# Kernel tuning notes

Measured on AMD Instinct MI355X. Metric: run time of the kernel, lower is better.

Reference implementation:

```python
import jax, jax.numpy as jnp
import numpy as np

B, C, D = 1024, 100000, 512
S_SCALE, MARGIN, EPS = 64.0, 0.5, 1e-7  # arcface defaults


def setup_inputs() -> dict:
    key = jax.random.key(0)
    kx, kl, kw = jax.random.split(key, 3)
    x = jax.random.normal(kx, (B, D), dtype=jnp.float32)
    labels = jax.random.randint(kl, (B,), 0, C, dtype=jnp.int64)
    # nn.Linear default init: U(-1/sqrt(fan_in), 1/sqrt(fan_in))
    bound = 1.0 / np.sqrt(D)
    W = jax.random.uniform(kw, (C, D), dtype=jnp.float32, minval=-bound, maxval=bound)
    return {"x": x, "labels": labels, "W": W}


def reference(x, labels, W):
    # L2-normalize features (W is NOT normalized in the original -- the
    # normalize loop there rebinds a local and is a no-op).
    xn = x / jnp.maximum(jnp.linalg.norm(x, axis=1, keepdims=True), 1e-12)
    wf = jnp.einsum('bd,cd->bc', xn, W)               # [B, C] cosine-like logits
    target = jnp.take_along_axis(wf, labels[:, None], axis=1)[:, 0]  # [B]
    # arcface: s * cos(acos(clamp(cos_theta)) + m)
    numerator = S_SCALE * jnp.cos(
        jnp.arccos(jnp.clip(target, -1.0 + EPS, 1.0 - EPS)) + MARGIN)
    # sum over excluded classes = full sum - label term
    excl_sum = jnp.sum(jnp.exp(S_SCALE * wf), axis=1) - jnp.exp(S_SCALE * target)
    L = numerator - jnp.log(jnp.exp(numerator) + excl_sum)
    return -jnp.mean(L)
```

## Files before the change

kernel.cpp:

```cpp
#include <hip/hip_runtime.h>
#include <hip/hip_bf16.h>
#include <math.h>

#define NB 1024
#define NC 100000
#define ND 512
#define SSCALE 64.0f
#define MMARGIN 0.5f

#define BM 128
#define BN 128
#define BK 64
#define NKS (ND / BK)
#define NRT (NB / BM)
#define NCT ((NC + BN - 1) / BN)
#define GRIDSZ (NRT * NCT)

typedef __bf16 bf16x8 __attribute__((ext_vector_type(8)));
typedef float f32x4 __attribute__((ext_vector_type(4)));

__device__ __forceinline__ void gload_lds16(const void* g, void* l) {
    __builtin_amdgcn_global_load_lds(
        (const __attribute__((address_space(1))) unsigned int*)g,
        (__attribute__((address_space(3))) unsigned int*)l, 16, 0, 0);
}


__global__ void prep_kernel(const float* __restrict__ x, __bf16* __restrict__ xnb) {
    const int row = blockIdx.x;
    const int tid = threadIdx.x;
    const float2 v = *reinterpret_cast<const float2*>(x + (size_t)row * ND + tid * 2);
    float ss = v.x * v.x + v.y * v.y;
#pragma unroll
    for (int m = 1; m < 64; m <<= 1) ss += __shfl_xor(ss, m);
    __shared__ float wsum[4];
    if ((tid & 63) == 0) wsum[tid >> 6] = ss;
    __syncthreads();
    const float tot = wsum[0] + wsum[1] + wsum[2] + wsum[3];
    const float inv = 1.0f / fmaxf(sqrtf(tot), 1e-12f);
    __bf16* dst = xnb + (size_t)row * ND + tid * 2;
    dst[0] = (__bf16)(v.x * inv);
    dst[1] = (__bf16)(v.y * inv);
}

__global__ void target_kernel(const __bf16* __restrict__ xnb, const float* __restrict__ Wg,
                              const int* __restrict__ labels, float* __restrict__ tgt) {
    const int wid  = threadIdx.x >> 6;
    const int lane = threadIdx.x & 63;
    const int row  = blockIdx.x * 4 + wid;
    const int lab  = labels[row];
    const int k    = lane * 8;
    const bf16x8 xv = *reinterpret_cast<const bf16x8*>(xnb + (size_t)row * ND + k);
    const float* wr = Wg + (size_t)lab * ND + k;
    const float4 w0 = *reinterpret_cast<const float4*>(wr);
    const float4 w1 = *reinterpret_cast<const float4*>(wr + 4);
    float s = (float)xv[0] * w0.x + (float)xv[1] * w0.y + (float)xv[2] * w0.z + (float)xv[3] * w0.w
            + (float)xv[4] * w1.x + (float)xv[5] * w1.y + (float)xv[6] * w1.z + (float)xv[7] * w1.w;
#pragma unroll
    for (int m = 1; m < 64; m <<= 1) s += __shfl_xor(s, m);
    if (lane == 0) tgt[row] = s;
}

__global__ __launch_bounds__(256, 3) void gemm_exp_kernel(const __bf16* __restrict__ xnb,
                                                          const float* __restrict__ Wg,
                                                          float* __restrict__ sums) {
    __shared__ char lds[49152];
    const int tid  = threadIdx.x;
    const int wid  = tid >> 6;
    const int lane = tid & 63;
    const int l15  = lane & 15;
    const int lhi  = lane >> 4;
    const int wr   = wid >> 1;
    const int wc   = wid & 1;

    const int logical = (blockIdx.x & 7) * (GRIDSZ / 8) + (blockIdx.x >> 3);
    const int rt = logical & 7;
    const int ct = logical >> 3;
    const int r0 = rt * BM;
    const int c0 = ct * BN;

    float4 bw[8];

    const int bcls = (tid >> 3);
    const int bqp  = tid & 7;

    auto loadB = [&](int t) {
#pragma unroll
        for (int l = 0; l < 4; ++l) {
            const int cls = l * 32 + bcls;
            const float* src = Wg + (size_t)(c0 + cls) * ND + t * BK + bqp * 8;
            if (c0 + cls < NC) {
                bw[l * 2]     = *reinterpret_cast<const float4*>(src);
                bw[l * 2 + 1] = *reinterpret_cast<const float4*>(src + 4);
            } else {
                bw[l * 2]     = make_float4(0.f, 0.f, 0.f, 0.f);
                bw[l * 2 + 1] = make_float4(0.f, 0.f, 0.f, 0.f);
            }
        }
    };
    auto writeB = [&]() {
#pragma unroll
        for (int l = 0; l < 4; ++l) {
            const int cls = l * 32 + bcls;
            struct alignas(16) bf8s { __bf16 h[8]; };
            bf8s h;
            const float4 v0 = bw[l * 2], v1 = bw[l * 2 + 1];
            h.h[0] = (__bf16)v0.x; h.h[1] = (__bf16)v0.y; h.h[2] = (__bf16)v0.z; h.h[3] = (__bf16)v0.w;
            h.h[4] = (__bf16)v1.x; h.h[5] = (__bf16)v1.y; h.h[6] = (__bf16)v1.z; h.h[7] = (__bf16)v1.w;
            const int byte = 32768 + cls * 128 + ((bqp ^ (cls & 7)) << 4);
            *reinterpret_cast<bf8s*>(lds + byte) = h;
        }
    };
    auto stageA = [&](int t, int buf) {
#pragma unroll
        for (int it = 0; it < 4; ++it) {
            const int row = it * 32 + wid * 8 + (lane >> 3);
            const int c   = lane & 7;
            const int lc  = c ^ (row & 7);
            const char* src = (const char*)xnb + (size_t)(r0 + row) * (ND * 2) + t * (BK * 2) + lc * 16;
            char* dstbase = lds + buf * 16384 + it * 4096 + wid * 1024;
            gload_lds16(src, dstbase);
        }
    };

    f32x4 acc[4][4] = {};

    auto compute = [&](int buf) {
#pragma unroll
        for (int kk = 0; kk < 2; ++kk) {
            bf16x8 a[4], b[4];
#pragma unroll
            for (int i = 0; i < 4; ++i) {
                const int r = wr * 64 + i * 16 + l15;
                const int byte = buf * 16384 + r * 128 + ((((kk << 2) | lhi) ^ (r & 7)) << 4);
                a[i] = *reinterpret_cast<const bf16x8*>(lds + byte);
            }
#pragma unroll
            for (int j = 0; j < 4; ++j) {
                const int cc = wc * 64 + j * 16 + l15;
                const int byte = 32768 + cc * 128 + ((((kk << 2) | lhi) ^ (cc & 7)) << 4);
                b[j] = *reinterpret_cast<const bf16x8*>(lds + byte);
            }
#pragma unroll
            for (int i = 0; i < 4; ++i)
#pragma unroll
                for (int j = 0; j < 4; ++j)
                    acc[i][j] = __builtin_amdgcn_mfma_f32_16x16x32_bf16(a[i], b[j], acc[i][j], 0, 0, 0);
        }
    };

    loadB(0);
    stageA(0, 0);
    writeB();
    __syncthreads();
    int cur = 0;
#pragma unroll 1
    for (int t = 0; t < NKS; ++t) {
        if (t + 1 < NKS) {
            loadB(t + 1);
            stageA(t + 1, cur ^ 1);
        }
        compute(cur);
        __syncthreads();
        if (t + 1 < NKS) writeB();
        __syncthreads();
        cur ^= 1;
    }

#pragma unroll
    for (int i = 0; i < 4; ++i) {
#pragma unroll
        for (int r = 0; r < 4; ++r) {
            float v = 0.f;
#pragma unroll
            for (int j = 0; j < 4; ++j) {
                const int c = c0 + wc * 64 + j * 16 + l15;
                v += (c < NC) ? __expf(SSCALE * acc[i][j][r]) : 0.f;
            }
            v += __shfl_xor(v, 1);
            v += __shfl_xor(v, 2);
            v += __shfl_xor(v, 4);
            v += __shfl_xor(v, 8);
            if (l15 == 0) {
                const int row = r0 + wr * 64 + i * 16 + lhi * 4 + r;
                atomicAdd(&sums[row], v);
            }
        }
    }
}

__global__ void finalize_kernel(const float* __restrict__ sums, const float* __restrict__ tgt,
                                float* __restrict__ out) {
    const int tid  = threadIdx.x;
    const int wid  = tid >> 6;
    const int lane = tid & 63;
    float t  = tgt[tid];
    const float se = sums[tid];
    t = fminf(fmaxf(t, -1.0f + 1e-7f), 1.0f - 1e-7f);
    const float numer = SSCALE * cosf(acosf(t) + MMARGIN);
    const float excl  = se - expf(SSCALE * t);
    float L = numer - logf(expf(numer) + excl);
#pragma unroll
    for (int m = 1; m < 64; m <<= 1) L += __shfl_xor(L, m);
    __shared__ float ws2[16];
    if (lane == 0) ws2[wid] = L;
    __syncthreads();
    if (tid == 0) {
        float tot = 0.f;
        for (int i = 0; i < 16; ++i) tot += ws2[i];
        out[0] = -(tot / (float)NB);
    }
}

extern "C" void kernel_launch(void* const* d_in, const int* in_sizes, int n_in,
                              void* d_out, int out_size, void* d_ws, size_t ws_size,
                              hipStream_t stream) {
    const float* x      = (const float*)d_in[0];
    const int*   labels = (const int*)d_in[1];
    const float* W      = (const float*)d_in[2];
    float* out = (float*)d_out;

    char* wsb = (char*)d_ws;
    __bf16* xnb  = (__bf16*)wsb;
    float*  sums = (float*)(wsb + (size_t)NB * ND * 2);
    float*  tgt  = sums + NB;

    hipMemsetAsync(sums, 0, NB * sizeof(float), stream);
    prep_kernel<<<NB, 256, 0, stream>>>(x, xnb);
    target_kernel<<<NB / 4, 256, 0, stream>>>(xnb, W, labels, tgt);
    gemm_exp_kernel<<<GRIDSZ, 256, 0, stream>>>(xnb, W, sums);
    finalize_kernel<<<1, 1024, 0, stream>>>(sums, tgt, out);
}
```

Measured before the change: 194.1 us.

## Enlarge GEMM row tile to 256 with 512 threads and double-buffered B

Doubles the row tile to 256 rows per block and runs it with 8 waves, while halving the K step to 32. Both the A and B tiles are now double-buffered in LDS, with a new XOR swizzle. This lets the main loop need only one barrier per iteration instead of two. Each W tile is now loaded and converted from fp32 to bf16 half as many times across the grid, cutting global traffic and conversion work on the dominant operand. The cost is more K iterations, larger blocks and possibly lower occupancy under the register and LDS limits.

```diff
diff --git a/kernel.cpp b/kernel.cpp
--- a/kernel.cpp
+++ b/kernel.cpp
@@ -8,13 +8,18 @@
 #define SSCALE 64.0f
 #define MMARGIN 0.5f
 
-#define BM 128
+#define BM 256
 #define BN 128
-#define BK 64
+#define BK 32
 #define NKS (ND / BK)
 #define NRT (NB / BM)
 #define NCT ((NC + BN - 1) / BN)
 #define GRIDSZ (NRT * NCT)
+
+#define ABASE 0
+#define ABUF  16384
+#define BBASE 32768
+#define BBUF  8192
 
 typedef __bf16 bf16x8 __attribute__((ext_vector_type(8)));
 typedef float f32x4 __attribute__((ext_vector_type(4)));
@@ -61,7 +66,7 @@
     if (lane == 0) tgt[row] = s;
 }
 
-__global__ __launch_bounds__(256, 3) void gemm_exp_kernel(const __bf16* __restrict__ xnb,
+__global__ __launch_bounds__(512, 4) void gemm_exp_kernel(const __bf16* __restrict__ xnb,
                                                           const float* __restrict__ Wg,
                                                           float* __restrict__ sums) {
     __shared__ char lds[49152];
@@ -74,97 +79,84 @@
     const int wc   = wid & 1;
 
     const int logical = (blockIdx.x & 7) * (GRIDSZ / 8) + (blockIdx.x >> 3);
-    const int rt = logical & 7;
-    const int ct = logical >> 3;
+    const int rt = logical & 3;
+    const int ct = logical >> 2;
     const int r0 = rt * BM;
     const int c0 = ct * BN;
 
-    float4 bw[8];
-
-    const int bcls = (tid >> 3);
-    const int bqp  = tid & 7;
-
+    const int bcls = tid >> 2;
+    const int bqk  = tid & 3;
+    const bool bok = (c0 + bcls) < NC;
+    float4 bw0, bw1;
     auto loadB = [&](int t) {
-#pragma unroll
-        for (int l = 0; l < 4; ++l) {
-            const int cls = l * 32 + bcls;
-            const float* src = Wg + (size_t)(c0 + cls) * ND + t * BK + bqp * 8;
-            if (c0 + cls < NC) {
-                bw[l * 2]     = *reinterpret_cast<const float4*>(src);
-                bw[l * 2 + 1] = *reinterpret_cast<const float4*>(src + 4);
-            } else {
-                bw[l * 2]     = make_float4(0.f, 0.f, 0.f, 0.f);
-                bw[l * 2 + 1] = make_float4(0.f, 0.f, 0.f, 0.f);
-            }
-        }
-    };
-    auto writeB = [&]() {
-#pragma unroll
-        for (int l = 0; l < 4; ++l) {
-            const int cls = l * 32 + bcls;
-            struct alignas(16) bf8s { __bf16 h[8]; };
-            bf8s h;
-            const float4 v0 = bw[l * 2], v1 = bw[l * 2 + 1];
-            h.h[0] = (__bf16)v0.x; h.h[1] = (__bf16)v0.y; h.h[2] = (__bf16)v0.z; h.h[3] = (__bf16)v0.w;
-            h.h[4] = (__bf16)v1.x; h.h[5] = (__bf16)v1.y; h.h[6] = (__bf16)v1.z; h.h[7] = (__bf16)v1.w;
-            const int byte = 32768 + cls * 128 + ((bqp ^ (cls & 7)) << 4);
-            *reinterpret_cast<bf8s*>(lds + byte) = h;
-        }
-    };
+        if (bok) {
+            const float* src = Wg + (size_t)(c0 + bcls) * ND + t * BK + bqk * 8;
+            bw0 = *reinterpret_cast<const float4*>(src);
+            bw1 = *reinterpret_cast<const float4*>(src + 4);
+        } else {
+            bw0 = make_float4(0.f, 0.f, 0.f, 0.f);
+            bw1 = bw0;
+        }
+    };
+    auto writeB = [&](int buf) {
+        struct alignas(16) bf8s { __bf16 h[8]; };
+        bf8s h;
+        h.h[0] = (__bf16)bw0.x; h.h[1] = (__bf16)bw0.y; h.h[2] = (__bf16)bw0.z; h.h[3] = (__bf16)bw0.w;
+        h.h[4] = (__bf16)bw1.x; h.h[5] = (__bf16)bw1.y; h.h[6] = (__bf16)bw1.z; h.h[7] = (__bf16)bw1.w;
+        const int ck = bqk ^ ((bcls >> 1) & 3);
+        *reinterpret_cast<bf8s*>(lds + BBASE + buf * BBUF + bcls * 64 + (ck << 4)) = h;
+    };
+
     auto stageA = [&](int t, int buf) {
 #pragma unroll
-        for (int it = 0; it < 4; ++it) {
-            const int row = it * 32 + wid * 8 + (lane >> 3);
-            const int c   = lane & 7;
-            const int lc  = c ^ (row & 7);
-            const char* src = (const char*)xnb + (size_t)(r0 + row) * (ND * 2) + t * (BK * 2) + lc * 16;
-            char* dstbase = lds + buf * 16384 + it * 4096 + wid * 1024;
-            gload_lds16(src, dstbase);
+        for (int s = 0; s < 2; ++s) {
+            const int lin = s * 8192 + wid * 1024 + (lane << 4);
+            const int row = lin >> 6;
+            const int cnk = (lin >> 4) & 3;
+            const int sc  = cnk ^ ((row >> 1) & 3);
+            const char* src = (const char*)xnb + (size_t)(r0 + row) * 1024 + t * 64 + sc * 16;
+            gload_lds16(src, lds + ABASE + buf * ABUF + s * 8192 + wid * 1024);
         }
     };
 
     f32x4 acc[4][4] = {};
 
     auto compute = [&](int buf) {
-#pragma unroll
-        for (int kk = 0; kk < 2; ++kk) {
-            bf16x8 a[4], b[4];
-#pragma unroll
-            for (int i = 0; i < 4; ++i) {
-                const int r = wr * 64 + i * 16 + l15;
-                const int byte = buf * 16384 + r * 128 + ((((kk << 2) | lhi) ^ (r & 7)) << 4);
-                a[i] = *reinterpret_cast<const bf16x8*>(lds + byte);
-            }
-#pragma unroll
-            for (int j = 0; j < 4; ++j) {
-                const int cc = wc * 64 + j * 16 + l15;
-                const int byte = 32768 + cc * 128 + ((((kk << 2) | lhi) ^ (cc & 7)) << 4);
-                b[j] = *reinterpret_cast<const bf16x8*>(lds + byte);
-            }
-#pragma unroll
-            for (int i = 0; i < 4; ++i)
-#pragma unroll
-                for (int j = 0; j < 4; ++j)
-                    acc[i][j] = __builtin_amdgcn_mfma_f32_16x16x32_bf16(a[i], b[j], acc[i][j], 0, 0, 0);
-        }
+        bf16x8 a[4], b[4];
+#pragma unroll
+        for (int i = 0; i < 4; ++i) {
+            const int r = wr * 64 + i * 16 + l15;
+            const int ck = lhi ^ ((r >> 1) & 3);
+            a[i] = *reinterpret_cast<const bf16x8*>(lds + ABASE + buf * ABUF + r * 64 + (ck << 4));
+        }
+#pragma unroll
+        for (int j = 0; j < 4; ++j) {
+            const int cls = wc * 64 + j * 16 + l15;
+            const int ck  = lhi ^ ((cls >> 1) & 3);
+            b[j] = *reinterpret_cast<const bf16x8*>(lds + BBASE + buf * BBUF + cls * 64 + (ck << 4));
+        }
+#pragma unroll
+        for (int i = 0; i < 4; ++i)
+#pragma unroll
+            for (int j = 0; j < 4; ++j)
+                acc[i][j] = __builtin_amdgcn_mfma_f32_16x16x32_bf16(a[i], b[j], acc[i][j], 0, 0, 0);
     };
 
     loadB(0);
     stageA(0, 0);
-    writeB();
+    writeB(0);
     __syncthreads();
-    int cur = 0;
+
 #pragma unroll 1
     for (int t = 0; t < NKS; ++t) {
+        const int buf = t & 1;
         if (t + 1 < NKS) {
             loadB(t + 1);
-            stageA(t + 1, cur ^ 1);
-        }
-        compute(cur);
+            stageA(t + 1, buf ^ 1);
+        }
+        compute(buf);
+        if (t + 1 < NKS) writeB(buf ^ 1);
         __syncthreads();
-        if (t + 1 < NKS) writeB();
-        __syncthreads();
-        cur ^= 1;
     }
 
 #pragma unroll
@@ -228,6 +220,6 @@
     hipMemsetAsync(sums, 0, NB * sizeof(float), stream);
     prep_kernel<<<NB, 256, 0, stream>>>(x, xnb);
     target_kernel<<<NB / 4, 256, 0, stream>>>(xnb, W, labels, tgt);
-    gemm_exp_kernel<<<GRIDSZ, 256, 0, stream>>>(xnb, W, sums);
+    gemm_exp_kernel<<<GRIDSZ, 512, 0, stream>>>(xnb, W, sums);
     finalize_kernel<<<1, 1024, 0, stream>>>(sums, tgt, out);
 }
```

Measured after the change: 238.1 us. +22.7%, slower.

## Double-buffer B tile in LDS and prefetch W two k-steps ahead

Applied to the files above, without the earlier changes.

Adds a second LDS buffer for the converted W tile, raising shared memory to 64KB, and keeps two register sets of W loads in flight so global loads run two k-steps ahead. The main loop is unrolled by two with fixed buffer indices. The two __syncthreads per step become a single hand-written s_waitcnt plus s_barrier that waits only for the A staging loads. The aim is to hide global-load latency and cut barrier stalls. In exchange, occupancy drops from 3 to 2 blocks per CU and register pressure rises.

```diff
diff --git a/kernel.cpp b/kernel.cpp
--- a/kernel.cpp
+++ b/kernel.cpp
@@ -15,6 +15,10 @@
 #define NRT (NB / BM)
 #define NCT ((NC + BN - 1) / BN)
 #define GRIDSZ (NRT * NCT)
+
+#define ABUF  16384
+#define BBASE 32768
+#define BBUF  16384
 
 typedef __bf16 bf16x8 __attribute__((ext_vector_type(8)));
 typedef float f32x4 __attribute__((ext_vector_type(4)));
@@ -61,10 +65,10 @@
     if (lane == 0) tgt[row] = s;
 }
 
-__global__ __launch_bounds__(256, 3) void gemm_exp_kernel(const __bf16* __restrict__ xnb,
+__global__ __launch_bounds__(256, 2) void gemm_exp_kernel(const __bf16* __restrict__ xnb,
                                                           const float* __restrict__ Wg,
                                                           float* __restrict__ sums) {
-    __shared__ char lds[49152];
+    __shared__ char lds[65536];
     const int tid  = threadIdx.x;
     const int wid  = tid >> 6;
     const int lane = tid & 63;
@@ -79,12 +83,9 @@
     const int r0 = rt * BM;
     const int c0 = ct * BN;
 
-    float4 bw[8];
-
-    const int bcls = (tid >> 3);
+    const int bcls = tid >> 3;
     const int bqp  = tid & 7;
-
-    auto loadB = [&](int t) {
+    auto loadB = [&](int t, float4 (&bw)[8]) {
 #pragma unroll
         for (int l = 0; l < 4; ++l) {
             const int cls = l * 32 + bcls;
@@ -98,7 +99,7 @@
             }
         }
     };
-    auto writeB = [&]() {
+    auto writeB = [&](float4 (&bw)[8], int buf) {
 #pragma unroll
         for (int l = 0; l < 4; ++l) {
             const int cls = l * 32 + bcls;
@@ -107,10 +108,11 @@
             const float4 v0 = bw[l * 2], v1 = bw[l * 2 + 1];
             h.h[0] = (__bf16)v0.x; h.h[1] = (__bf16)v0.y; h.h[2] = (__bf16)v0.z; h.h[3] = (__bf16)v0.w;
             h.h[4] = (__bf16)v1.x; h.h[5] = (__bf16)v1.y; h.h[6] = (__bf16)v1.z; h.h[7] = (__bf16)v1.w;
-            const int byte = 32768 + cls * 128 + ((bqp ^ (cls & 7)) << 4);
+            const int byte = BBASE + buf * BBUF + cls * 128 + ((bqp ^ (cls & 7)) << 4);
             *reinterpret_cast<bf8s*>(lds + byte) = h;
         }
     };
+
     auto stageA = [&](int t, int buf) {
 #pragma unroll
         for (int it = 0; it < 4; ++it) {
@@ -118,8 +120,7 @@
             const int c   = lane & 7;
             const int lc  = c ^ (row & 7);
             const char* src = (const char*)xnb + (size_t)(r0 + row) * (ND * 2) + t * (BK * 2) + lc * 16;
-            char* dstbase = lds + buf * 16384 + it * 4096 + wid * 1024;
-            gload_lds16(src, dstbase);
+            gload_lds16(src, lds + buf * ABUF + it * 4096 + wid * 1024);
         }
     };
 
@@ -132,13 +133,13 @@
 #pragma unroll
             for (int i = 0; i < 4; ++i) {
                 const int r = wr * 64 + i * 16 + l15;
-                const int byte = buf * 16384 + r * 128 + ((((kk << 2) | lhi) ^ (r & 7)) << 4);
+                const int byte = buf * ABUF + r * 128 + ((((kk << 2) | lhi) ^ (r & 7)) << 4);
                 a[i] = *reinterpret_cast<const bf16x8*>(lds + byte);
             }
 #pragma unroll
             for (int j = 0; j < 4; ++j) {
                 const int cc = wc * 64 + j * 16 + l15;
-                const int byte = 32768 + cc * 128 + ((((kk << 2) | lhi) ^ (cc & 7)) << 4);
+                const int byte = BBASE + buf * BBUF + cc * 128 + ((((kk << 2) | lhi) ^ (cc & 7)) << 4);
                 b[j] = *reinterpret_cast<const bf16x8*>(lds + byte);
             }
 #pragma unroll
@@ -149,22 +150,34 @@
         }
     };
 
-    loadB(0);
+    float4 bw0[8], bw1[8];
+
+    loadB(0, bw0);
     stageA(0, 0);
-    writeB();
-    __syncthreads();
-    int cur = 0;
+    loadB(1, bw1);
+    writeB(bw0, 0);
+    asm volatile("s_waitcnt vmcnt(8) lgkmcnt(0)\n\ts_barrier" ::: "memory");
+
 #pragma unroll 1
-    for (int t = 0; t < NKS; ++t) {
-        if (t + 1 < NKS) {
-            loadB(t + 1);
-            stageA(t + 1, cur ^ 1);
-        }
-        compute(cur);
-        __syncthreads();
-        if (t + 1 < NKS) writeB();
-        __syncthreads();
-        cur ^= 1;
+    for (int tt = 0; tt < NKS; tt += 2) {
+        {
+            const int t = tt;
+            if (t + 1 < NKS) stageA(t + 1, 1);
+            if (t + 2 < NKS) loadB(t + 2, bw0);
+            compute(0);
+            if (t + 1 < NKS) writeB(bw1, 1);
+            if (t + 2 < NKS) asm volatile("s_waitcnt vmcnt(8) lgkmcnt(0)\n\ts_barrier" ::: "memory");
+            else             asm volatile("s_waitcnt vmcnt(0) lgkmcnt(0)\n\ts_barrier" ::: "memory");
+        }
+        {
+            const int t = tt + 1;
+            if (t + 1 < NKS) stageA(t + 1, 0);
+            if (t + 2 < NKS) loadB(t + 2, bw1);
+            compute(1);
+            if (t + 1 < NKS) writeB(bw0, 0);
+            if (t + 2 < NKS) asm volatile("s_waitcnt vmcnt(8) lgkmcnt(0)\n\ts_barrier" ::: "memory");
+            else             asm volatile("s_waitcnt vmcnt(0) lgkmcnt(0)\n\ts_barrier" ::: "memory");
+        }
     }
 
 #pragma unroll
```

Result: slower. 225.5 us (+16.2%).

## Pre-convert W to bf16 and stream B operands directly into registers

Applied to the files above, without the earlier changes.

Adds a separate kernel that converts W to bf16 once per call into workspace. The GEMM then loads B fragments straight from global memory into registers, skipping the LDS staging. The GEMM moves to 512 threads with 8 waves, each owning 64x32 of the tile, and uses a hand-built double-buffered pipeline with explicit vmcnt waits and barriers. This aims to halve the W bytes the GEMM reads repeatedly and to remove the LDS write/sync of B. The cost is an extra full pass over W (read fp32, write bf16) and dependence on workspace size.

```diff
diff --git a/kernel.cpp b/kernel.cpp
--- a/kernel.cpp
+++ b/kernel.cpp
@@ -24,6 +24,9 @@
         (const __attribute__((address_space(1))) unsigned int*)g,
         (__attribute__((address_space(3))) unsigned int*)l, 16, 0, 0);
 }
+__device__ __forceinline__ void bar_vm4() { asm volatile("s_waitcnt vmcnt(4)\ns_barrier" ::: "memory"); }
+__device__ __forceinline__ void bar_vm8() { asm volatile("s_waitcnt vmcnt(8)\ns_barrier" ::: "memory"); }
+__device__ __forceinline__ void bar_vm0() { asm volatile("s_waitcnt vmcnt(0)\ns_barrier" ::: "memory"); }
 
 
 __global__ void prep_kernel(const float* __restrict__ x, __bf16* __restrict__ xnb) {
@@ -61,17 +64,29 @@
     if (lane == 0) tgt[row] = s;
 }
 
-__global__ __launch_bounds__(256, 3) void gemm_exp_kernel(const __bf16* __restrict__ xnb,
-                                                          const float* __restrict__ Wg,
+__global__ void cvtw_kernel(const float* __restrict__ W, __bf16* __restrict__ Wbf) {
+    const size_t gid = (size_t)blockIdx.x * 256 + threadIdx.x;
+    const float4 v0 = *reinterpret_cast<const float4*>(W + gid * 8);
+    const float4 v1 = *reinterpret_cast<const float4*>(W + gid * 8 + 4);
+    bf16x8 h;
+    h[0] = (__bf16)v0.x; h[1] = (__bf16)v0.y; h[2] = (__bf16)v0.z; h[3] = (__bf16)v0.w;
+    h[4] = (__bf16)v1.x; h[5] = (__bf16)v1.y; h[6] = (__bf16)v1.z; h[7] = (__bf16)v1.w;
+    *reinterpret_cast<bf16x8*>(Wbf + gid * 8) = h;
+}
+
+template<int BMODE>
+__global__ __launch_bounds__(512, 4) void gemm_exp_kernel(const __bf16* __restrict__ xnb,
+                                                          const void* __restrict__ Bsrc,
                                                           float* __restrict__ sums) {
-    __shared__ char lds[49152];
+    constexpr int NBL = (BMODE == 0) ? 4 : 8;
+    __shared__ char lds[32768];
     const int tid  = threadIdx.x;
     const int wid  = tid >> 6;
     const int lane = tid & 63;
     const int l15  = lane & 15;
     const int lhi  = lane >> 4;
-    const int wr   = wid >> 1;
-    const int wc   = wid & 1;
+    const int wr2  = wid >> 2;
+    const int wc4  = wid & 3;
 
     const int logical = (blockIdx.x & 7) * (GRIDSZ / 8) + (blockIdx.x >> 3);
     const int rt = logical & 7;
@@ -79,92 +94,109 @@
     const int r0 = rt * BM;
     const int c0 = ct * BN;
 
-    float4 bw[8];
-
-    const int bcls = (tid >> 3);
-    const int bqp  = tid & 7;
-
-    auto loadB = [&](int t) {
-#pragma unroll
-        for (int l = 0; l < 4; ++l) {
-            const int cls = l * 32 + bcls;
-            const float* src = Wg + (size_t)(c0 + cls) * ND + t * BK + bqp * 8;
-            if (c0 + cls < NC) {
-                bw[l * 2]     = *reinterpret_cast<const float4*>(src);
-                bw[l * 2 + 1] = *reinterpret_cast<const float4*>(src + 4);
-            } else {
-                bw[l * 2]     = make_float4(0.f, 0.f, 0.f, 0.f);
-                bw[l * 2 + 1] = make_float4(0.f, 0.f, 0.f, 0.f);
-            }
-        }
+    const __bf16* bpb[2];
+    const float*  bpf[2];
+#pragma unroll
+    for (int j = 0; j < 2; ++j) {
+        int cls = c0 + wc4 * 32 + j * 16 + l15;
+        cls = cls < NC ? cls : NC - 1;
+        if (BMODE == 0) bpb[j] = (const __bf16*)Bsrc + (size_t)cls * ND + lhi * 8;
+        else            bpf[j] = (const float*)Bsrc + (size_t)cls * ND + lhi * 8;
+    }
+
+    bf16x8 SA[2][2], SB[2][2];
+    float4 RA[2][2][2], RB[2][2][2];
+
+    auto loadB = [&](int t, bf16x8 (&S)[2][2], float4 (&R)[2][2][2]) {
+#pragma unroll
+        for (int j = 0; j < 2; ++j)
+#pragma unroll
+            for (int kk = 0; kk < 2; ++kk) {
+                if constexpr (BMODE == 0) {
+                    S[j][kk] = *reinterpret_cast<const bf16x8*>(bpb[j] + t * 64 + kk * 32);
+                } else {
+                    R[j][kk][0] = *reinterpret_cast<const float4*>(bpf[j] + t * 64 + kk * 32);
+                    R[j][kk][1] = *reinterpret_cast<const float4*>(bpf[j] + t * 64 + kk * 32 + 4);
+                }
+            }
     };
-    auto writeB = [&]() {
-#pragma unroll
-        for (int l = 0; l < 4; ++l) {
-            const int cls = l * 32 + bcls;
-            struct alignas(16) bf8s { __bf16 h[8]; };
-            bf8s h;
-            const float4 v0 = bw[l * 2], v1 = bw[l * 2 + 1];
-            h.h[0] = (__bf16)v0.x; h.h[1] = (__bf16)v0.y; h.h[2] = (__bf16)v0.z; h.h[3] = (__bf16)v0.w;
-            h.h[4] = (__bf16)v1.x; h.h[5] = (__bf16)v1.y; h.h[6] = (__bf16)v1.z; h.h[7] = (__bf16)v1.w;
-            const int byte = 32768 + cls * 128 + ((bqp ^ (cls & 7)) << 4);
-            *reinterpret_cast<bf8s*>(lds + byte) = h;
+
+    auto stageA = [&](int t, int buf) {
+#pragma unroll
+        for (int s = 0; s < 2; ++s) {
+            const int lin = s * 8192 + tid * 16;
+            const int row = lin >> 7;
+            const int dc  = (lin >> 4) & 7;
+            const int lc  = dc ^ (row & 7);
+            const char* src = (const char*)xnb + (size_t)(r0 + row) * 1024 + t * 128 + lc * 16;
+            gload_lds16(src, lds + buf * 16384 + s * 8192 + wid * 1024);
         }
     };
-    auto stageA = [&](int t, int buf) {
-#pragma unroll
-        for (int it = 0; it < 4; ++it) {
-            const int row = it * 32 + wid * 8 + (lane >> 3);
-            const int c   = lane & 7;
-            const int lc  = c ^ (row & 7);
-            const char* src = (const char*)xnb + (size_t)(r0 + row) * (ND * 2) + t * (BK * 2) + lc * 16;
-            char* dstbase = lds + buf * 16384 + it * 4096 + wid * 1024;
-            gload_lds16(src, dstbase);
+
+    f32x4 acc[4][2] = {};
+
+    auto compute = [&](int buf, bf16x8 (&S)[2][2], float4 (&R)[2][2][2]) {
+#pragma unroll
+        for (int kk = 0; kk < 2; ++kk) {
+            bf16x8 a[4], b[2];
+#pragma unroll
+            for (int i = 0; i < 4; ++i) {
+                const int r  = wr2 * 64 + i * 16 + l15;
+                const int ck = (kk << 2) | lhi;
+                a[i] = *reinterpret_cast<const bf16x8*>(
+                    lds + buf * 16384 + r * 128 + ((ck ^ (r & 7)) << 4));
+            }
+#pragma unroll
+            for (int j = 0; j < 2; ++j) {
+                if constexpr (BMODE == 0) {
+                    b[j] = S[j][kk];
+                } else {
+                    const float4 lo = R[j][kk][0], hi = R[j][kk][1];
+                    bf16x8 t8;
+                    t8[0] = (__bf16)lo.x; t8[1] = (__bf16)lo.y; t8[2] = (__bf16)lo.z; t8[3] = (__bf16)lo.w;
+                    t8[4] = (__bf16)hi.x; t8[5] = (__bf16)hi.y; t8[6] = (__bf16)hi.z; t8[7] = (__bf16)hi.w;
+                    b[j] = t8;
+                }
+            }
+#pragma unroll
+            for (int i = 0; i < 4; ++i)
+#pragma unroll
+                for (int j = 0; j < 2; ++j)
+                    acc[i][j] = __builtin_amdgcn_mfma_f32_16x16x32_bf16(a[i], b[j], acc[i][j], 0, 0, 0);
         }
     };
 
-    f32x4 acc[4][4] = {};
-
-    auto compute = [&](int buf) {
-#pragma unroll
-        for (int kk = 0; kk < 2; ++kk) {
-            bf16x8 a[4], b[4];
-#pragma unroll
-            for (int i = 0; i < 4; ++i) {
-                const int r = wr * 64 + i * 16 + l15;
-                const int byte = buf * 16384 + r * 128 + ((((kk << 2) | lhi) ^ (r & 7)) << 4);
-                a[i] = *reinterpret_cast<const bf16x8*>(lds + byte);
-            }
-#pragma unroll
-            for (int j = 0; j < 4; ++j) {
-                const int cc = wc * 64 + j * 16 + l15;
-                const int byte = 32768 + cc * 128 + ((((kk << 2) | lhi) ^ (cc & 7)) << 4);
-                b[j] = *reinterpret_cast<const bf16x8*>(lds + byte);
-            }
-#pragma unroll
-            for (int i = 0; i < 4; ++i)
-#pragma unroll
-                for (int j = 0; j < 4; ++j)
-                    acc[i][j] = __builtin_amdgcn_mfma_f32_16x16x32_bf16(a[i], b[j], acc[i][j], 0, 0, 0);
-        }
-    };
-
-    loadB(0);
+    loadB(0, SA, RA);
     stageA(0, 0);
-    writeB();
-    __syncthreads();
-    int cur = 0;
-#pragma unroll 1
-    for (int t = 0; t < NKS; ++t) {
-        if (t + 1 < NKS) {
-            loadB(t + 1);
-            stageA(t + 1, cur ^ 1);
-        }
-        compute(cur);
-        __syncthreads();
-        if (t + 1 < NKS) writeB();
-        __syncthreads();
-        cur ^= 1;
+    __builtin_amdgcn_sched_barrier(0);
+    loadB(1, SB, RB);
+    __builtin_amdgcn_sched_barrier(0);
+    if constexpr (NBL == 4) bar_vm4(); else bar_vm8();
+
+#pragma unroll
+    for (int tt = 0; tt < NKS; tt += 2) {
+        {   const int t = tt;
+            if (t + 1 < NKS) stageA(t + 1, (t + 1) & 1);
+            __builtin_amdgcn_sched_barrier(0);
+            compute(t & 1, SA, RA);
+            if (t + 2 < NKS) loadB(t + 2, SA, RA);
+            __builtin_amdgcn_sched_barrier(0);
+            if (t + 1 < NKS) {
+                if (t + 2 < NKS) { if constexpr (NBL == 4) bar_vm4(); else bar_vm8(); }
+                else bar_vm0();
+            }
+        }
+        {   const int t = tt + 1;
+            if (t + 1 < NKS) stageA(t + 1, (t + 1) & 1);
+            __builtin_amdgcn_sched_barrier(0);
+            compute(t & 1, SB, RB);
+            if (t + 2 < NKS) loadB(t + 2, SB, RB);
+            __builtin_amdgcn_sched_barrier(0);
+            if (t + 1 < NKS) {
+                if (t + 2 < NKS) { if constexpr (NBL == 4) bar_vm4(); else bar_vm8(); }
+                else bar_vm0();
+            }
+        }
     }
 
 #pragma unroll
@@ -173,8 +205,8 @@
         for (int r = 0; r < 4; ++r) {
             float v = 0.f;
 #pragma unroll
-            for (int j = 0; j < 4; ++j) {
-                const int c = c0 + wc * 64 + j * 16 + l15;
+            for (int j = 0; j < 2; ++j) {
+                const int c = c0 + wc4 * 32 + j * 16 + l15;
                 v += (c < NC) ? __expf(SSCALE * acc[i][j][r]) : 0.f;
             }
             v += __shfl_xor(v, 1);
@@ -182,7 +214,7 @@
             v += __shfl_xor(v, 4);
             v += __shfl_xor(v, 8);
             if (l15 == 0) {
-                const int row = r0 + wr * 64 + i * 16 + lhi * 4 + r;
+                const int row = r0 + wr2 * 64 + i * 16 + lhi * 4 + r;
                 atomicAdd(&sums[row], v);
             }
         }
@@ -222,12 +254,19 @@
 
     char* wsb = (char*)d_ws;
     __bf16* xnb  = (__bf16*)wsb;
-    float*  sums = (float*)(wsb + (size_t)NB * ND * 2);
-    float*  tgt  = sums + NB;
+    float*  sums = (float*)(wsb + 1048576);
+    float*  tgt  = (float*)(wsb + 1052672);
+    __bf16* Wbf  = (__bf16*)(wsb + 1056768);
+    const size_t WS_NEED = 1056768ull + (size_t)NC * ND * 2;
 
     hipMemsetAsync(sums, 0, NB * sizeof(float), stream);
     prep_kernel<<<NB, 256, 0, stream>>>(x, xnb);
     target_kernel<<<NB / 4, 256, 0, stream>>>(xnb, W, labels, tgt);
-    gemm_exp_kernel<<<GRIDSZ, 256, 0, stream>>>(xnb, W, sums);
+    if (ws_size >= WS_NEED) {
+        cvtw_kernel<<<(NC * ND) / (256 * 8), 256, 0, stream>>>(W, Wbf);
+        gemm_exp_kernel<0><<<GRIDSZ, 512, 0, stream>>>(xnb, Wbf, sums);
+    } else {
+        gemm_exp_kernel<1><<<GRIDSZ, 512, 0, stream>>>(xnb, W, sums);
+    }
     finalize_kernel<<<1, 1024, 0, stream>>>(sums, tgt, out);
 }
```

Result: slower. 411.6 us (+112.1%).
